# Optimization experiments

Hardware: AMD Instinct MI355X
Metric: run time of the kernel (lower is better)

## Reference

```python
import jax, jax.numpy as jnp
import numpy as np

BN_EPS = 1e-5


def haar_dwt2(x):
    # pywt.dwt2(img,'haar'/'db1') -> cA,(cH,cV,cD) with Haar filters lo=[1,1]/sqrt2, hi=[1,-1]/sqrt2.
    # cA=(a+b+c+d)/2, cH('da')=(a+b-c-d)/2, cV('ad')=(a-b+c-d)/2, cD=(a-b-c+d)/2
    # where a=x[2i,2j], b=x[2i,2j+1], c=x[2i+1,2j], d=x[2i+1,2j+1].
    B, C, H, W = x.shape
    xr = x.reshape(B, C, H // 2, 2, W // 2, 2)
    a = xr[:, :, :, 0, :, 0]
    b = xr[:, :, :, 0, :, 1]
    c = xr[:, :, :, 1, :, 0]
    d = xr[:, :, :, 1, :, 1]
    ll = (a + b + c + d) * 0.5
    lh = (a + b - c - d) * 0.5
    hl = (a - b + c - d) * 0.5
    hh = (a - b - c + d) * 0.5
    # interleave per input channel: [LL, LH, HL, HH] -> [B, 4C, H/2, W/2]
    return jnp.stack([ll, lh, hl, hh], axis=2).reshape(B, C * 4, H // 2, W // 2)


def conv_transpose2d(x, w, b):
    # torch ConvTranspose2d(k=4, s=2, p=1); w: [Cin, Cout, 4, 4] (torch layout)
    wk = jnp.flip(w, (-2, -1)).transpose(1, 0, 2, 3)  # [Cout, Cin, 4, 4]
    y = jax.lax.conv_general_dilated(
        x, wk, window_strides=(1, 1), padding=((2, 2), (2, 2)),
        lhs_dilation=(2, 2), dimension_numbers=('NCHW', 'OIHW', 'NCHW'))
    return y + b[None, :, None, None]


def bn_relu(x, g, beta, m, v):
    inv = g * jax.lax.rsqrt(v + BN_EPS)
    return jax.nn.relu((x - m[None, :, None, None]) * inv[None, :, None, None]
                       + beta[None, :, None, None])


def setup_inputs() -> dict:
    key = jax.random.key(0)
    ks = jax.random.split(key, 8)
    Cin, emb_dim = 3, 96
    half = emb_dim // 2  # 48
    B, H, W = 16, 256, 256
    x = jax.random.normal(ks[0], (B, Cin, H, W), dtype=jnp.float32)

    def convT_params(k, cin, cout):
        k1, k2 = jax.random.split(k)
        fan = float(cin * 16)
        w = jax.random.normal(k1, (cin, cout, 4, 4), dtype=jnp.float32) / np.sqrt(fan)
        b = jax.random.normal(k2, (cout,), dtype=jnp.float32) * 0.01
        return w, b

    def bn_params(k, c):
        k1, k2, k3 = jax.random.split(k, 3)
        g = 1.0 + 0.1 * jax.random.normal(k1, (c,), dtype=jnp.float32)
        beta = 0.1 * jax.random.normal(k2, (c,), dtype=jnp.float32)
        m = 0.1 * jax.random.normal(k3, (c,), dtype=jnp.float32)
        v = jnp.ones((c,), dtype=jnp.float32)
        return g, beta, m, v

    w1, b1 = convT_params(ks[1], 4 * Cin, half)
    g1, beta1, m1, v1 = bn_params(ks[2], half)
    w2a, b2a = convT_params(ks[3], 16 * Cin, half)
    g2a, beta2a, m2a, v2a = bn_params(ks[4], half)
    w2b, b2b = convT_params(ks[5], half, half)
    g2b, beta2b, m2b, v2b = bn_params(ks[6], half)

    return dict(x=x, w1=w1, b1=b1, g1=g1, beta1=beta1, m1=m1, v1=v1,
                w2a=w2a, b2a=b2a, g2a=g2a, beta2a=beta2a, m2a=m2a, v2a=v2a,
                w2b=w2b, b2b=b2b, g2b=g2b, beta2b=beta2b, m2b=m2b, v2b=v2b)


def reference(x, w1, b1, g1, beta1, m1, v1,
              w2a, b2a, g2a, beta2a, m2a, v2a,
              w2b, b2b, g2b, beta2b, m2b, v2b):
    x_l1 = haar_dwt2(x)                                  # [B, 4Cin, H/2, W/2]
    out = bn_relu(conv_transpose2d(x_l1, w1, b1), g1, beta1, m1, v1)   # [B, half, H, W]
    x_l2 = haar_dwt2(x_l1)                               # [B, 16Cin, H/4, W/4]
    out2 = bn_relu(conv_transpose2d(x_l2, w2a, b2a), g2a, beta2a, m2a, v2a)
    out2 = bn_relu(conv_transpose2d(out2, w2b, b2b), g2b, beta2b, m2b, v2b)  # [B, half, H, W]
    return jnp.concatenate([out, out2], axis=1)          # [B, emb_dim, H, W]
```

## Files before the change

### kernel.cpp

```cpp
#include <hip/hip_runtime.h>

typedef short s16x8 __attribute__((ext_vector_type(8)));
typedef float f32x4 __attribute__((ext_vector_type(4)));
typedef unsigned short u16;

#define BN_EPS 1e-5f

__device__ __forceinline__ u16 f2bf(float f) {
  union { float f; unsigned u; } v; v.f = f;
  unsigned r = (v.u + 0x7fffu + ((v.u >> 16) & 1u)) >> 16;
  return (u16)r;
}
__device__ __forceinline__ float bf2f(u16 u) {
  union { unsigned u; float f; } v; v.u = ((unsigned)u) << 16; return v.f;
}

__global__ __launch_bounds__(256) void dwt_f32_kernel(
    const float* __restrict__ in, u16* __restrict__ out,
    int B, int C, int H, int W)
{
  int H2 = H >> 1, W2 = W >> 1;
  long total = (long)B * C * H2 * W2;
  long idx = (long)blockIdx.x * 256 + threadIdx.x;
  if (idx >= total) return;
  int w2 = (int)(idx % W2); long t = idx / W2;
  int h2 = (int)(t % H2); t /= H2;
  int c = (int)(t % C); int b = (int)(t / C);
  const float* p = in + (((long)(b * C + c) * H + 2 * h2) * W + 2 * w2);
  float2 u = *(const float2*)p;
  float2 v = *(const float2*)(p + W);
  float a = u.x, bb = u.y, cc = v.x, dd = v.y;
  float ll = (a + bb + cc + dd) * 0.5f;
  float lh = (a + bb - cc - dd) * 0.5f;
  float hl = (a - bb + cc - dd) * 0.5f;
  float hh = (a - bb - cc + dd) * 0.5f;
  long cs = (long)H2 * W2;
  u16* q = out + ((long)(b * 4 * C + 4 * c)) * cs + (long)h2 * W2 + w2;
  q[0] = f2bf(ll); q[cs] = f2bf(lh); q[2 * cs] = f2bf(hl); q[3 * cs] = f2bf(hh);
}

__global__ __launch_bounds__(256) void dwt_bf16_kernel(
    const u16* __restrict__ in, u16* __restrict__ out,
    int B, int C, int H, int W)
{
  int H2 = H >> 1, W2 = W >> 1;
  long total = (long)B * C * H2 * W2;
  long idx = (long)blockIdx.x * 256 + threadIdx.x;
  if (idx >= total) return;
  int w2 = (int)(idx % W2); long t = idx / W2;
  int h2 = (int)(t % H2); t /= H2;
  int c = (int)(t % C); int b = (int)(t / C);
  const u16* p = in + (((long)(b * C + c) * H + 2 * h2) * W + 2 * w2);
  unsigned r0 = *(const unsigned*)p;
  unsigned r1 = *(const unsigned*)(p + W);
  float a = bf2f((u16)(r0 & 0xffff)), bb = bf2f((u16)(r0 >> 16));
  float cc = bf2f((u16)(r1 & 0xffff)), dd = bf2f((u16)(r1 >> 16));
  float ll = (a + bb + cc + dd) * 0.5f;
  float lh = (a + bb - cc - dd) * 0.5f;
  float hl = (a - bb + cc - dd) * 0.5f;
  float hh = (a - bb - cc + dd) * 0.5f;
  long cs = (long)H2 * W2;
  u16* q = out + ((long)(b * 4 * C + 4 * c)) * cs + (long)h2 * W2 + w2;
  q[0] = f2bf(ll); q[cs] = f2bf(lh); q[2 * cs] = f2bf(hl); q[3 * cs] = f2bf(hh);
}

__global__ __launch_bounds__(256) void setup_kernel(
    const float* __restrict__ w, const float* __restrict__ bias,
    const float* __restrict__ g, const float* __restrict__ be,
    const float* __restrict__ mu, const float* __restrict__ var,
    u16* __restrict__ Bp, float* __restrict__ bnp,
    int CIN, int CIP, int KSTEPS)
{
  int e = blockIdx.x * 256 + threadIdx.x;
  if (e < 48) {
    float iv = g[e] * rsqrtf(var[e] + BN_EPS);
    bnp[e] = iv;
    bnp[48 + e] = (bias[e] - mu[e]) * iv + be[e];
  }
  int total = 4 * KSTEPS * 1536;
  if (e >= total) return;
  int j = e & 7;
  int l = (e >> 3) & 63;
  int nt = (e >> 9) % 3;
  int sp = e / 1536;
  int s = sp % KSTEPS;
  int p = sp / KSTEPS;
  int py = p >> 1, px = p & 1;
  int n = nt * 16 + (l & 15);
  int k = s * 32 + (l >> 4) * 8 + j;
  int tap = k / CIP, ci = k % CIP;
  int kh = 2 * (tap >> 1) + 1 - py;
  int kw = 2 * (tap & 1) + 1 - px;
  float v = (ci < CIN) ? w[((ci * 48 + n) * 4 + kh) * 4 + kw] : 0.f;
  Bp[e] = f2bf(v);
}

template<int CIN, int CIP, int HIN, int WIN, bool OBF16>
__global__ __launch_bounds__(256, 2) void convt_mfma(
    const u16* __restrict__ in,
    const u16* __restrict__ Bp,
    const float* __restrict__ bnp,
    void* __restrict__ outv, int outc, int obase)
{
  constexpr int KSTEPS = CIP / 8;
  constexpr int IT = 18;
  constexpr int HOUT = 2 * HIN, WOUT = 2 * WIN;
  __shared__ __align__(16) u16 in_lds[IT * IT * CIP];
  __shared__ __align__(16) float out_lds[48 * 4 * 32];

  const int tid = threadIdx.x;
  const int n = blockIdx.z;
  const int qY0 = blockIdx.y * 16;
  const int qX0 = blockIdx.x * 16;

  {
    constexpr int NTASK = CIP * IT * 2;
    for (int t = tid; t < NTASK; t += 256) {
      int half = t & 1;
      int rowid = t >> 1;
      int ci = rowid / IT;
      int y = rowid - ci * IT;
      int ih = qY0 - 1 + y;
      bool rowok = (CIP == CIN || ci < CIN) && ((unsigned)ih < (unsigned)HIN);
      const u16* gsrc = in + (((long)n * CIN + ci) * HIN + ih) * WIN + qX0 + 8 * half;
      s16x8 v = {0, 0, 0, 0, 0, 0, 0, 0};
      if (rowok) v = *(const s16x8*)gsrc;
      int xh = half ? 17 : 0;
      int iwh = qX0 - 1 + xh;
      u16 hv = 0;
      if (rowok && (unsigned)iwh < (unsigned)WIN) hv = gsrc[half ? 8 : -1];
      int base_yx = y * IT;
      #pragma unroll
      for (int j = 0; j < 8; ++j) {
        int x = 1 + 8 * half + j;
        int rot = 8 * ((x >> 2) & 3);
        if (rot >= CIP) rot -= CIP;
        int cr = ci + rot;
        if (cr >= CIP) cr -= CIP;
        in_lds[(base_yx + x) * CIP + cr] = (u16)v[j];
      }
      {
        int rot = 8 * ((xh >> 2) & 3);
        if (rot >= CIP) rot -= CIP;
        int cr = ci + rot;
        if (cr >= CIP) cr -= CIP;
        in_lds[(base_yx + xh) * CIP + cr] = hv;
      }
    }
  }

  const int wid = tid >> 6, lane = tid & 63;
  const int py = wid >> 1, px = wid & 1;
  const int g = lane >> 4, qx = lane & 15;

  s16x8 bf[KSTEPS][3];
  const s16x8* bpp = (const s16x8*)Bp + (wid * KSTEPS * 3) * 64 + lane;
  #pragma unroll
  for (int s = 0; s < KSTEPS; ++s)
    #pragma unroll
    for (int nt = 0; nt < 3; ++nt)
      bf[s][nt] = bpp[(s * 3 + nt) * 64];

  float4 inv4[3], sh4[3];
  #pragma unroll
  for (int nt = 0; nt < 3; ++nt) {
    inv4[nt] = *(const float4*)&bnp[nt * 16 + 4 * g];
    sh4[nt]  = *(const float4*)&bnp[48 + nt * 16 + 4 * g];
  }

  int abase[KSTEPS];
  #pragma unroll
  for (int s = 0; s < KSTEPS; ++s) {
    int k0 = s * 32 + g * 8;
    int tap = k0 / CIP, ci0 = k0 - tap * CIP;
    int ty = tap >> 1, tx = tap & 1;
    int y = 1 + py - ty;
    int x = qx + 1 + px - tx;
    int rot = 8 * ((x >> 2) & 3);
    if (rot >= CIP) rot -= CIP;
    int cr = ci0 + rot;
    if (cr >= CIP) cr -= CIP;
    abase[s] = (y * IT + x) * CIP + cr;
  }

  __syncthreads();

  for (int mc = 0; mc < 4; ++mc) {
    f32x4 acc[4][3];
    #pragma unroll
    for (int mt = 0; mt < 4; ++mt)
      #pragma unroll
      for (int nt = 0; nt < 3; ++nt)
        acc[mt][nt] = f32x4{0.f, 0.f, 0.f, 0.f};

    #pragma unroll
    for (int s = 0; s < KSTEPS; ++s) {
      #pragma unroll
      for (int mt = 0; mt < 4; ++mt) {
        const int qy = mc * 4 + mt;
        s16x8 a = *(const s16x8*)&in_lds[abase[s] + qy * (IT * CIP)];
        #pragma unroll
        for (int nt = 0; nt < 3; ++nt)
          acc[mt][nt] = __builtin_amdgcn_mfma_f32_16x16x32_bf16(
              bf[s][nt], a, acc[mt][nt], 0, 0, 0);
      }
    }

    #pragma unroll
    for (int c2 = 0; c2 < 2; ++c2) {
      __syncthreads();
      #pragma unroll
      for (int mtl = 0; mtl < 2; ++mtl) {
        const int mt = 2 * c2 + mtl;
        const int ohl = 2 * mtl + py;
        #pragma unroll
        for (int nt = 0; nt < 3; ++nt) {
          #pragma unroll
          for (int r = 0; r < 4; ++r) {
            const int co_l = nt * 16 + 4 * g + r;
            float iv = ((const float*)&inv4[nt])[r];
            float sv = ((const float*)&sh4[nt])[r];
            float val = fmaxf(acc[mt][nt][r] * iv + sv, 0.f);
            out_lds[(co_l * 4 + ohl) * 32 + 2 * qx + px] = val;
          }
        }
      }
      __syncthreads();
      const int oh_base = 2 * (qY0 + 4 * mc + 2 * c2);
      #pragma unroll
      for (int u = 0; u < 6; ++u) {
        int e = u * 256 + tid;
        int owq = e & 7, ohl = (e >> 3) & 3, co_l = e >> 5;
        float4 vv = *(const float4*)&out_lds[(co_l * 4 + ohl) * 32 + 4 * owq];
        long off = (((long)(n * outc + obase + co_l) * HOUT + oh_base + ohl) * WOUT)
                   + 2 * qX0 + 4 * owq;
        if (OBF16) {
          u16 h0 = f2bf(vv.x), h1 = f2bf(vv.y), h2 = f2bf(vv.z), h3 = f2bf(vv.w);
          unsigned lo = (unsigned)h0 | ((unsigned)h1 << 16);
          unsigned hi = (unsigned)h2 | ((unsigned)h3 << 16);
          uint2 pk; pk.x = lo; pk.y = hi;
          *(uint2*)((u16*)outv + off) = pk;
        } else {
          *(float4*)((float*)outv + off) = vv;
        }
      }
    }
  }
}

extern "C" void kernel_launch(void* const* d_in, const int* in_sizes, int n_in,
                              void* d_out, int out_size, void* d_ws, size_t ws_size,
                              hipStream_t stream) {
  const float* x    = (const float*)d_in[0];
  const float* w1   = (const float*)d_in[1];
  const float* b1   = (const float*)d_in[2];
  const float* g1   = (const float*)d_in[3];
  const float* be1  = (const float*)d_in[4];
  const float* m1   = (const float*)d_in[5];
  const float* v1   = (const float*)d_in[6];
  const float* w2a  = (const float*)d_in[7];
  const float* b2a  = (const float*)d_in[8];
  const float* g2a  = (const float*)d_in[9];
  const float* be2a = (const float*)d_in[10];
  const float* m2a  = (const float*)d_in[11];
  const float* v2a  = (const float*)d_in[12];
  const float* w2b  = (const float*)d_in[13];
  const float* b2b  = (const float*)d_in[14];
  const float* g2b  = (const float*)d_in[15];
  const float* be2b = (const float*)d_in[16];
  const float* m2b  = (const float*)d_in[17];
  const float* v2b  = (const float*)d_in[18];

  float* out = (float*)d_out;
  char* ws = (char*)d_ws;
  u16* xl1  = (u16*)ws;
  u16* xl2  = (u16*)(ws + 6291456);
  u16* o2a  = (u16*)(ws + 12582912);
  u16* Bp1  = (u16*)(ws + 37748736);
  u16* Bp2a = (u16*)(ws + 37773312);
  u16* Bp2b = (u16*)(ws + 37847040);
  float* bnp1  = (float*)(ws + 37920768);
  float* bnp2a = (float*)(ws + 37921152);
  float* bnp2b = (float*)(ws + 37921536);

  setup_kernel<<<48, 256, 0, stream>>>(w1, b1, g1, be1, m1, v1, Bp1, bnp1, 12, 16, 2);
  setup_kernel<<<144, 256, 0, stream>>>(w2a, b2a, g2a, be2a, m2a, v2a, Bp2a, bnp2a, 48, 48, 6);
  setup_kernel<<<144, 256, 0, stream>>>(w2b, b2b, g2b, be2b, m2b, v2b, Bp2b, bnp2b, 48, 48, 6);

  dwt_f32_kernel<<<3072, 256, 0, stream>>>(x, xl1, 16, 3, 256, 256);
  dwt_bf16_kernel<<<3072, 256, 0, stream>>>(xl1, xl2, 16, 12, 128, 128);

  convt_mfma<12, 16, 128, 128, false><<<dim3(8, 8, 16), 256, 0, stream>>>(
      xl1, Bp1, bnp1, out, 96, 0);
  convt_mfma<48, 48, 64, 64, true><<<dim3(4, 4, 16), 256, 0, stream>>>(
      xl2, Bp2a, bnp2a, o2a, 48, 0);
  convt_mfma<48, 48, 128, 128, false><<<dim3(8, 8, 16), 256, 0, stream>>>(
      o2a, Bp2b, bnp2b, out, 96, 48);
}
```

Baseline: 138.7 us.

## Fuse DWT levels and setup kernels, retile convT blocks to wide rows

Merges the two Haar DWT kernels into one that reads 4x4 fp32 patches and emits both level-1 and level-2 bands, removing the bf16 re-read of xl1. The three weight-packing launches become a single 2D-grid launch. The transposed-conv kernel switches from 16x16 input tiles to 64x4 tiles, so each output row segment is 256 bytes wide. This gives longer contiguous global stores, which are now nontemporal for fp32 output. The epilogue is restaged through a differently shaped LDS buffer, and halo loads now happen only on the edge segments.

```diff
diff --git a/kernel.cpp b/kernel.cpp
--- a/kernel.cpp
+++ b/kernel.cpp
@@ -15,63 +15,60 @@
   union { unsigned u; float f; } v; v.u = ((unsigned)u) << 16; return v.f;
 }
 
-__global__ __launch_bounds__(256) void dwt_f32_kernel(
-    const float* __restrict__ in, u16* __restrict__ out,
-    int B, int C, int H, int W)
+__global__ __launch_bounds__(256) void dwt_fused_kernel(
+    const float* __restrict__ x, u16* __restrict__ xl1, u16* __restrict__ xl2)
 {
-  int H2 = H >> 1, W2 = W >> 1;
-  long total = (long)B * C * H2 * W2;
-  long idx = (long)blockIdx.x * 256 + threadIdx.x;
-  if (idx >= total) return;
-  int w2 = (int)(idx % W2); long t = idx / W2;
-  int h2 = (int)(t % H2); t /= H2;
-  int c = (int)(t % C); int b = (int)(t / C);
-  const float* p = in + (((long)(b * C + c) * H + 2 * h2) * W + 2 * w2);
-  float2 u = *(const float2*)p;
-  float2 v = *(const float2*)(p + W);
-  float a = u.x, bb = u.y, cc = v.x, dd = v.y;
-  float ll = (a + bb + cc + dd) * 0.5f;
-  float lh = (a + bb - cc - dd) * 0.5f;
-  float hl = (a - bb + cc - dd) * 0.5f;
-  float hh = (a - bb - cc + dd) * 0.5f;
-  long cs = (long)H2 * W2;
-  u16* q = out + ((long)(b * 4 * C + 4 * c)) * cs + (long)h2 * W2 + w2;
-  q[0] = f2bf(ll); q[cs] = f2bf(lh); q[2 * cs] = f2bf(hl); q[3 * cs] = f2bf(hh);
-}
-
-__global__ __launch_bounds__(256) void dwt_bf16_kernel(
-    const u16* __restrict__ in, u16* __restrict__ out,
-    int B, int C, int H, int W)
-{
-  int H2 = H >> 1, W2 = W >> 1;
-  long total = (long)B * C * H2 * W2;
-  long idx = (long)blockIdx.x * 256 + threadIdx.x;
-  if (idx >= total) return;
-  int w2 = (int)(idx % W2); long t = idx / W2;
-  int h2 = (int)(t % H2); t /= H2;
-  int c = (int)(t % C); int b = (int)(t / C);
-  const u16* p = in + (((long)(b * C + c) * H + 2 * h2) * W + 2 * w2);
-  unsigned r0 = *(const unsigned*)p;
-  unsigned r1 = *(const unsigned*)(p + W);
-  float a = bf2f((u16)(r0 & 0xffff)), bb = bf2f((u16)(r0 >> 16));
-  float cc = bf2f((u16)(r1 & 0xffff)), dd = bf2f((u16)(r1 >> 16));
-  float ll = (a + bb + cc + dd) * 0.5f;
-  float lh = (a + bb - cc - dd) * 0.5f;
-  float hl = (a - bb + cc - dd) * 0.5f;
-  float hh = (a - bb - cc + dd) * 0.5f;
-  long cs = (long)H2 * W2;
-  u16* q = out + ((long)(b * 4 * C + 4 * c)) * cs + (long)h2 * W2 + w2;
-  q[0] = f2bf(ll); q[cs] = f2bf(lh); q[2 * cs] = f2bf(hl); q[3 * cs] = f2bf(hh);
-}
-
-__global__ __launch_bounds__(256) void setup_kernel(
+  int idx = blockIdx.x * 256 + threadIdx.x;
+  int w4 = idx & 63; int t = idx >> 6;
+  int h4 = t & 63; t >>= 6;
+  int c = t % 3; int b = t / 3;
+  const float* p = x + (((long)(b * 3 + c) * 256 + 4 * h4) * 256 + 4 * w4);
+  float4 r[4];
+  r[0] = *(const float4*)p;
+  r[1] = *(const float4*)(p + 256);
+  r[2] = *(const float4*)(p + 512);
+  r[3] = *(const float4*)(p + 768);
+  float rows[4][4] = {{r[0].x, r[0].y, r[0].z, r[0].w},
+                      {r[1].x, r[1].y, r[1].z, r[1].w},
+                      {r[2].x, r[2].y, r[2].z, r[2].w},
+                      {r[3].x, r[3].y, r[3].z, r[3].w}};
+  float sb[4][2][2];
+  #pragma unroll
+  for (int qy = 0; qy < 2; ++qy)
+    #pragma unroll
+    for (int qx = 0; qx < 2; ++qx) {
+      float a = rows[2 * qy][2 * qx],     bb = rows[2 * qy][2 * qx + 1];
+      float cc = rows[2 * qy + 1][2 * qx], dd = rows[2 * qy + 1][2 * qx + 1];
+      sb[0][qy][qx] = (a + bb + cc + dd) * 0.5f;
+      sb[1][qy][qx] = (a + bb - cc - dd) * 0.5f;
+      sb[2][qy][qx] = (a - bb + cc - dd) * 0.5f;
+      sb[3][qy][qx] = (a - bb - cc + dd) * 0.5f;
+    }
+  #pragma unroll
+  for (int s = 0; s < 4; ++s)
+    #pragma unroll
+    for (int qy = 0; qy < 2; ++qy) {
+      unsigned pk = (unsigned)f2bf(sb[s][qy][0]) | ((unsigned)f2bf(sb[s][qy][1]) << 16);
+      *(unsigned*)&xl1[(((long)(b * 12 + 4 * c + s) * 128) + 2 * h4 + qy) * 128 + 2 * w4] = pk;
+    }
+  #pragma unroll
+  for (int s = 0; s < 4; ++s) {
+    float a = sb[s][0][0], bb = sb[s][0][1], cc = sb[s][1][0], dd = sb[s][1][1];
+    float o[4] = {(a + bb + cc + dd) * 0.5f, (a + bb - cc - dd) * 0.5f,
+                  (a - bb + cc - dd) * 0.5f, (a - bb - cc + dd) * 0.5f};
+    #pragma unroll
+    for (int s2 = 0; s2 < 4; ++s2)
+      xl2[(((long)(b * 48 + (4 * c + s) * 4 + s2) * 64) + h4) * 64 + w4] = f2bf(o[s2]);
+  }
+}
+
+__device__ void setup_one(
     const float* __restrict__ w, const float* __restrict__ bias,
     const float* __restrict__ g, const float* __restrict__ be,
     const float* __restrict__ mu, const float* __restrict__ var,
     u16* __restrict__ Bp, float* __restrict__ bnp,
-    int CIN, int CIP, int KSTEPS)
+    int CIN, int CIP, int KSTEPS, int e)
 {
-  int e = blockIdx.x * 256 + threadIdx.x;
   if (e < 48) {
     float iv = g[e] * rsqrtf(var[e] + BN_EPS);
     bnp[e] = iv;
@@ -95,6 +92,20 @@
   Bp[e] = f2bf(v);
 }
 
+__global__ __launch_bounds__(256) void setup_all_kernel(
+    const float* w1, const float* b1, const float* g1, const float* be1,
+    const float* m1, const float* v1, u16* Bp1, float* bnp1,
+    const float* w2a, const float* b2a, const float* g2a, const float* be2a,
+    const float* m2a, const float* v2a, u16* Bp2a, float* bnp2a,
+    const float* w2b, const float* b2b, const float* g2b, const float* be2b,
+    const float* m2b, const float* v2b, u16* Bp2b, float* bnp2b)
+{
+  int e = blockIdx.x * 256 + threadIdx.x;
+  if (blockIdx.y == 0)      setup_one(w1, b1, g1, be1, m1, v1, Bp1, bnp1, 12, 16, 2, e);
+  else if (blockIdx.y == 1) setup_one(w2a, b2a, g2a, be2a, m2a, v2a, Bp2a, bnp2a, 48, 48, 6, e);
+  else                      setup_one(w2b, b2b, g2b, be2b, m2b, v2b, Bp2b, bnp2b, 48, 48, 6, e);
+}
+
 template<int CIN, int CIP, int HIN, int WIN, bool OBF16>
 __global__ __launch_bounds__(256, 2) void convt_mfma(
     const u16* __restrict__ in,
@@ -103,43 +114,43 @@
     void* __restrict__ outv, int outc, int obase)
 {
   constexpr int KSTEPS = CIP / 8;
-  constexpr int IT = 18;
+  constexpr int ITX = 66, ITY = 6;
   constexpr int HOUT = 2 * HIN, WOUT = 2 * WIN;
-  __shared__ __align__(16) u16 in_lds[IT * IT * CIP];
-  __shared__ __align__(16) float out_lds[48 * 4 * 32];
+  __shared__ __align__(16) u16 in_lds[ITX * ITY * CIP];
+  __shared__ __align__(16) float out_lds[32 * 2 * 128];
 
   const int tid = threadIdx.x;
   const int n = blockIdx.z;
-  const int qY0 = blockIdx.y * 16;
-  const int qX0 = blockIdx.x * 16;
+  const int qY0 = blockIdx.y * 4;
+  const int qX0 = blockIdx.x * 64;
 
   {
-    constexpr int NTASK = CIP * IT * 2;
+    constexpr int NTASK = CIP * ITY * 8;
     for (int t = tid; t < NTASK; t += 256) {
-      int half = t & 1;
-      int rowid = t >> 1;
-      int ci = rowid / IT;
-      int y = rowid - ci * IT;
+      int seg = t & 7;
+      int rowid = t >> 3;
+      int ci = rowid / ITY;
+      int y = rowid - ci * ITY;
       int ih = qY0 - 1 + y;
       bool rowok = (CIP == CIN || ci < CIN) && ((unsigned)ih < (unsigned)HIN);
-      const u16* gsrc = in + (((long)n * CIN + ci) * HIN + ih) * WIN + qX0 + 8 * half;
+      const u16* gsrc = in + (((long)n * CIN + ci) * HIN + ih) * WIN + qX0 + 8 * seg;
       s16x8 v = {0, 0, 0, 0, 0, 0, 0, 0};
       if (rowok) v = *(const s16x8*)gsrc;
-      int xh = half ? 17 : 0;
-      int iwh = qX0 - 1 + xh;
-      u16 hv = 0;
-      if (rowok && (unsigned)iwh < (unsigned)WIN) hv = gsrc[half ? 8 : -1];
-      int base_yx = y * IT;
+      int base_yx = y * ITX;
       #pragma unroll
       for (int j = 0; j < 8; ++j) {
-        int x = 1 + 8 * half + j;
-        int rot = 8 * ((x >> 2) & 3);
+        int xx = 1 + 8 * seg + j;
+        int rot = 8 * ((xx >> 2) & 3);
         if (rot >= CIP) rot -= CIP;
         int cr = ci + rot;
         if (cr >= CIP) cr -= CIP;
-        in_lds[(base_yx + x) * CIP + cr] = (u16)v[j];
-      }
-      {
+        in_lds[(base_yx + xx) * CIP + cr] = (u16)v[j];
+      }
+      if (seg == 0 || seg == 7) {
+        int xh = (seg == 0) ? 0 : 65;
+        int iwh = qX0 - 1 + xh;
+        u16 hv = 0;
+        if (rowok && (unsigned)iwh < (unsigned)WIN) hv = gsrc[(seg == 0) ? -1 : 8];
         int rot = 8 * ((xh >> 2) & 3);
         if (rot >= CIP) rot -= CIP;
         int cr = ci + rot;
@@ -175,12 +186,12 @@
     int tap = k0 / CIP, ci0 = k0 - tap * CIP;
     int ty = tap >> 1, tx = tap & 1;
     int y = 1 + py - ty;
-    int x = qx + 1 + px - tx;
-    int rot = 8 * ((x >> 2) & 3);
+    int xx = qx + 1 + px - tx;
+    int rot = 8 * ((xx >> 2) & 3);
     if (rot >= CIP) rot -= CIP;
     int cr = ci0 + rot;
     if (cr >= CIP) cr -= CIP;
-    abase[s] = (y * IT + x) * CIP + cr;
+    abase[s] = (y * ITX + xx) * CIP + cr;
   }
 
   __syncthreads();
@@ -197,8 +208,7 @@
     for (int s = 0; s < KSTEPS; ++s) {
       #pragma unroll
       for (int mt = 0; mt < 4; ++mt) {
-        const int qy = mc * 4 + mt;
-        s16x8 a = *(const s16x8*)&in_lds[abase[s] + qy * (IT * CIP)];
+        s16x8 a = *(const s16x8*)&in_lds[abase[s] + (mc * ITX + mt * 16) * CIP];
         #pragma unroll
         for (int nt = 0; nt < 3; ++nt)
           acc[mt][nt] = __builtin_amdgcn_mfma_f32_16x16x32_bf16(
@@ -207,41 +217,47 @@
     }
 
     #pragma unroll
-    for (int c2 = 0; c2 < 2; ++c2) {
+    for (int sc = 0; sc < 2; ++sc) {
+      const int ntlo = (sc == 0) ? 0 : 2;
+      const int ntn  = (sc == 0) ? 2 : 1;
+      const int coBase = ntlo * 16;
       __syncthreads();
       #pragma unroll
-      for (int mtl = 0; mtl < 2; ++mtl) {
-        const int mt = 2 * c2 + mtl;
-        const int ohl = 2 * mtl + py;
-        #pragma unroll
-        for (int nt = 0; nt < 3; ++nt) {
+      for (int ntl = 0; ntl < 2; ++ntl) {
+        if (ntl < ntn) {
+          const int nt = ntlo + ntl;
           #pragma unroll
-          for (int r = 0; r < 4; ++r) {
-            const int co_l = nt * 16 + 4 * g + r;
-            float iv = ((const float*)&inv4[nt])[r];
-            float sv = ((const float*)&sh4[nt])[r];
-            float val = fmaxf(acc[mt][nt][r] * iv + sv, 0.f);
-            out_lds[(co_l * 4 + ohl) * 32 + 2 * qx + px] = val;
+          for (int mt = 0; mt < 4; ++mt) {
+            #pragma unroll
+            for (int r = 0; r < 4; ++r) {
+              const int co_rel = ntl * 16 + 4 * g + r;
+              float iv = ((const float*)&inv4[nt])[r];
+              float sv = ((const float*)&sh4[nt])[r];
+              float val = fmaxf(acc[mt][nt][r] * iv + sv, 0.f);
+              out_lds[(co_rel * 2 + py) * 128 + 2 * (mt * 16 + qx) + px] = val;
+            }
           }
         }
       }
       __syncthreads();
-      const int oh_base = 2 * (qY0 + 4 * mc + 2 * c2);
-      #pragma unroll
-      for (int u = 0; u < 6; ++u) {
-        int e = u * 256 + tid;
-        int owq = e & 7, ohl = (e >> 3) & 3, co_l = e >> 5;
-        float4 vv = *(const float4*)&out_lds[(co_l * 4 + ohl) * 32 + 4 * owq];
-        long off = (((long)(n * outc + obase + co_l) * HOUT + oh_base + ohl) * WOUT)
-                   + 2 * qX0 + 4 * owq;
-        if (OBF16) {
-          u16 h0 = f2bf(vv.x), h1 = f2bf(vv.y), h2 = f2bf(vv.z), h3 = f2bf(vv.w);
-          unsigned lo = (unsigned)h0 | ((unsigned)h1 << 16);
-          unsigned hi = (unsigned)h2 | ((unsigned)h3 << 16);
-          uint2 pk; pk.x = lo; pk.y = hi;
-          *(uint2*)((u16*)outv + off) = pk;
-        } else {
-          *(float4*)((float*)outv + off) = vv;
+      const int nIter = ntn * 4;
+      #pragma unroll
+      for (int u = 0; u < 8; ++u) {
+        if (u < nIter) {
+          int e = u * 256 + tid;
+          int ow4 = e & 31, row = e >> 5;
+          int co_l = coBase + (row >> 1), ohp = row & 1;
+          f32x4 vv = *(const f32x4*)&out_lds[row * 128 + 4 * ow4];
+          long off = (((long)(n * outc + obase + co_l) * HOUT + 2 * (qY0 + mc) + ohp) * WOUT)
+                     + 2 * qX0 + 4 * ow4;
+          if (OBF16) {
+            unsigned lo = (unsigned)f2bf(vv.x) | ((unsigned)f2bf(vv.y) << 16);
+            unsigned hi = (unsigned)f2bf(vv.z) | ((unsigned)f2bf(vv.w) << 16);
+            uint2 pk; pk.x = lo; pk.y = hi;
+            *(uint2*)((u16*)outv + off) = pk;
+          } else {
+            __builtin_nontemporal_store(vv, (f32x4*)((float*)outv + off));
+          }
         }
       }
     }
@@ -283,17 +299,17 @@
   float* bnp2a = (float*)(ws + 37921152);
   float* bnp2b = (float*)(ws + 37921536);
 
-  setup_kernel<<<48, 256, 0, stream>>>(w1, b1, g1, be1, m1, v1, Bp1, bnp1, 12, 16, 2);
-  setup_kernel<<<144, 256, 0, stream>>>(w2a, b2a, g2a, be2a, m2a, v2a, Bp2a, bnp2a, 48, 48, 6);
-  setup_kernel<<<144, 256, 0, stream>>>(w2b, b2b, g2b, be2b, m2b, v2b, Bp2b, bnp2b, 48, 48, 6);
-
-  dwt_f32_kernel<<<3072, 256, 0, stream>>>(x, xl1, 16, 3, 256, 256);
-  dwt_bf16_kernel<<<3072, 256, 0, stream>>>(xl1, xl2, 16, 12, 128, 128);
-
-  convt_mfma<12, 16, 128, 128, false><<<dim3(8, 8, 16), 256, 0, stream>>>(
+  setup_all_kernel<<<dim3(144, 3), 256, 0, stream>>>(
+      w1, b1, g1, be1, m1, v1, Bp1, bnp1,
+      w2a, b2a, g2a, be2a, m2a, v2a, Bp2a, bnp2a,
+      w2b, b2b, g2b, be2b, m2b, v2b, Bp2b, bnp2b);
+
+  dwt_fused_kernel<<<768, 256, 0, stream>>>(x, xl1, xl2);
+
+  convt_mfma<12, 16, 128, 128, false><<<dim3(2, 32, 16), 256, 0, stream>>>(
       xl1, Bp1, bnp1, out, 96, 0);
-  convt_mfma<48, 48, 64, 64, true><<<dim3(4, 4, 16), 256, 0, stream>>>(
+  convt_mfma<48, 48, 64, 64, true><<<dim3(1, 16, 16), 256, 0, stream>>>(
       xl2, Bp2a, bnp2a, o2a, 48, 0);
-  convt_mfma<48, 48, 128, 128, false><<<dim3(8, 8, 16), 256, 0, stream>>>(
+  convt_mfma<48, 48, 128, 128, false><<<dim3(2, 32, 16), 256, 0, stream>>>(
       o2a, Bp2b, bnp2b, out, 96, 48);
 }
```

Result: faster. 130.9 us (-5.6%).
